# Optimization experiments

Hardware: AMD Instinct MI355X
Metric: run time of the kernel (lower is better)

## Reference

```python
import jax, jax.numpy as jnp
import numpy as np

NW = 64        # n_waveshapers
CE = 128       # control_embedding_size
W = 16         # shaping_fn_size (width)
OC = 1         # out_channels
EPS = 1e-5
SLOPE = 0.01   # LeakyReLU negative slope


def _layer_norm_c(x, g, b):
    # layer norm over channel axis of [B, C, T] (TimeDistributedLayerNorm)
    mu = jnp.mean(x, axis=1, keepdims=True)
    var = jnp.var(x, axis=1, keepdims=True)
    xn = (x - mu) * jax.lax.rsqrt(var + EPS)
    return xn * g[None, :, None] + b[None, :, None]


def _linear_interp(x, out_len):
    # torch F.interpolate(mode='linear', align_corners=False) on [B, C, L]
    L = x.shape[-1]
    scale = L / out_len
    pos = (jnp.arange(out_len, dtype=x.dtype) + 0.5) * scale - 0.5
    pos = jnp.clip(pos, 0.0, L - 1)
    i0 = jnp.floor(pos).astype(jnp.int32)
    i1 = jnp.minimum(i0 + 1, L - 1)
    frac = (pos - i0.astype(x.dtype))
    return x[..., i0] * (1.0 - frac) + x[..., i1] * frac


def setup_inputs() -> dict:
    key = jax.random.key(0)
    ks = jax.random.split(key, 32)
    B, T, TC = 4, 65536, 1024
    s_ce = 1.0 / np.sqrt(CE)
    inp = {
        'exciter': jax.random.normal(ks[0], (B, NW, T), jnp.float32),
        'control_embedding': jax.random.normal(ks[1], (B, CE, TC), jnp.float32),
        # TimeDistributedMLP (depth=4): three CE->CE convs + final CE->4*NW
        'mlp_w0': jax.random.normal(ks[2], (CE, CE), jnp.float32) * s_ce,
        'mlp_b0': jnp.zeros((CE,), jnp.float32),
        'ln0_g': jnp.ones((CE,), jnp.float32),
        'ln0_b': jnp.zeros((CE,), jnp.float32),
        'mlp_w1': jax.random.normal(ks[3], (CE, CE), jnp.float32) * s_ce,
        'mlp_b1': jnp.zeros((CE,), jnp.float32),
        'ln1_g': jnp.ones((CE,), jnp.float32),
        'ln1_b': jnp.zeros((CE,), jnp.float32),
        'mlp_w2': jax.random.normal(ks[4], (CE, CE), jnp.float32) * s_ce,
        'mlp_b2': jnp.zeros((CE,), jnp.float32),
        'ln2_g': jnp.ones((CE,), jnp.float32),
        'ln2_b': jnp.zeros((CE,), jnp.float32),
        'mlp_w3': jax.random.normal(ks[5], (4 * NW, CE), jnp.float32) * s_ce,
        'mlp_b3': jnp.zeros((4 * NW,), jnp.float32),
        # TrainableNonlinearity: input_scale + grouped k=1 convs (per-channel MLPs)
        'input_scale': jax.random.normal(ks[6], (1, NW, 1), jnp.float32) * 10.0,
        'sf_w0': jax.random.normal(ks[7], (NW, W), jnp.float32),            # 1 -> W per group
        'sf_b0': jnp.zeros((NW, W), jnp.float32),
        'sf_w1': jax.random.normal(ks[8], (NW, W, W), jnp.float32) / np.sqrt(W),  # W -> W per group
        'sf_b1': jnp.zeros((NW, W), jnp.float32),
        'sf_w2': jax.random.normal(ks[9], (NW, W), jnp.float32) / np.sqrt(W),     # W -> 1 per group
        'sf_b2': jnp.zeros((NW,), jnp.float32),
        # mixer conv1d NW -> OC, k=1
        'mix_w': jax.random.normal(ks[10], (OC, NW), jnp.float32) / np.sqrt(NW),
        'mix_b': jnp.zeros((OC,), jnp.float32),
    }
    return inp


def reference(exciter, control_embedding,
              mlp_w0, mlp_b0, ln0_g, ln0_b,
              mlp_w1, mlp_b1, ln1_g, ln1_b,
              mlp_w2, mlp_b2, ln2_g, ln2_b,
              mlp_w3, mlp_b3,
              input_scale, sf_w0, sf_b0, sf_w1, sf_b1, sf_w2, sf_b2,
              mix_w, mix_b):
    T = exciter.shape[-1]

    # --- TimeDistributedMLP: (Conv1x1 -> LN(channels) -> LeakyReLU) x3 -> Conv1x1
    h = jnp.einsum('bct,oc->bot', control_embedding, mlp_w0) + mlp_b0[None, :, None]
    h = jax.nn.leaky_relu(_layer_norm_c(h, ln0_g, ln0_b), SLOPE)
    h = jnp.einsum('bct,oc->bot', h, mlp_w1) + mlp_b1[None, :, None]
    h = jax.nn.leaky_relu(_layer_norm_c(h, ln1_g, ln1_b), SLOPE)
    h = jnp.einsum('bct,oc->bot', h, mlp_w2) + mlp_b2[None, :, None]
    h = jax.nn.leaky_relu(_layer_norm_c(h, ln2_g, ln2_b), SLOPE)
    film = jnp.einsum('bct,oc->bot', h, mlp_w3) + mlp_b3[None, :, None]  # [B, 4*NW, TC]

    # upsample control params to audio rate
    film = _linear_interp(film, T)  # [B, 4*NW, T]
    gamma_i, beta_i, gamma_n, beta_n = jnp.split(film, 4, axis=1)

    # FiLM waveshaping index
    x = gamma_i * exciter + beta_i  # [B, NW, T]

    # TrainableNonlinearity: per-channel 1->W->W->1 MLP, Sine activations
    x = input_scale * x
    h0 = jnp.sin(x[:, :, None, :] * sf_w0[None, :, :, None] + sf_b0[None, :, :, None])  # [B,NW,W,T]
    h1 = jnp.sin(jnp.einsum('bcit,coi->bcot', h0, sf_w1) + sf_b1[None, :, :, None])     # [B,NW,W,T]
    x = jnp.sin(jnp.einsum('bcit,ci->bct', h1, sf_w2) + sf_b2[None, :, None])           # [B,NW,T]

    # FiLM normalising coeff
    x = gamma_n * x + beta_n

    # nearest upsample x4 then 1x1 mixer conv
    x = jnp.repeat(x, 4, axis=-1)  # [B, NW, 4T]
    out = jnp.einsum('bct,oc->bot', x, mix_w) + mix_b[None, :, None]  # [B, OC, 4T]
    return out
```

## Files before the change

### kernel.cpp

```cpp
#include <hip/hip_runtime.h>
#include <stdint.h>

#define NB 4
#define NWS 64
#define TT 65536
#define TCC 1024
#define CEE 128
#define WW 16

#define INV2PI 0.15915494309189535f

#define OFF_FILM  0
#define OFF_W0S   (OFF_FILM + NB*256*TCC)
#define OFF_B0S   (OFF_W0S + 1024)
#define OFF_B1S   (OFF_B0S + 1024)
#define OFF_B2S   (OFF_B1S + 1024)
#define OFF_MIX   (OFF_B2S + 64)
#define OFF_AFRAG (OFF_MIX + 64)
#define OFF_A2F   (OFF_AFRAG + 8192)
#define OFF_PART  (OFF_A2F + 8192)

typedef _Float16 half4_t __attribute__((ext_vector_type(4)));
typedef float f32x4_t __attribute__((ext_vector_type(4)));

__device__ __forceinline__ float sinrev(float r) {
#if __has_builtin(__builtin_amdgcn_fractf) && __has_builtin(__builtin_amdgcn_sinf)
  return __builtin_amdgcn_sinf(__builtin_amdgcn_fractf(r));
#else
  float fr = r - floorf(r);
  return __sinf(fr * 6.283185307179586f);
#endif
}

__global__ __launch_bounds__(256) void k_prep(
    const float* __restrict__ iscale,
    const float* __restrict__ w0, const float* __restrict__ b0,
    const float* __restrict__ w1, const float* __restrict__ b1,
    const float* __restrict__ w2, const float* __restrict__ b2,
    const float* __restrict__ mixw,
    float* __restrict__ ws) {
  int i = blockIdx.x * 256 + threadIdx.x;
  if (i < NWS * WW) {
    int n = i / WW;
    ws[OFF_W0S + i] = w0[i] * iscale[n] * INV2PI;
    ws[OFF_B0S + i] = b0[i] * INV2PI;
    ws[OFF_B1S + i] = b1[i] * INV2PI;
  }
  if (i < NWS) {
    ws[OFF_B2S + i] = b2[i] * INV2PI;
    ws[OFF_MIX + i] = mixw[i];
  }
  if (i < NWS * 64) {
    int n = i >> 6, l = i & 63;
    int m = l & 15, k0 = (l >> 4) * 4;
    union { uint2 u; half4_t h; } cv;
    #pragma unroll
    for (int j = 0; j < 4; ++j)
      cv.h[j] = (_Float16)(w1[(n * 16 + m) * 16 + k0 + j] * INV2PI);
    ((uint2*)(ws + OFF_AFRAG))[i] = cv.u;
    union { uint2 u; half4_t h; } c2;
    #pragma unroll
    for (int j = 0; j < 4; ++j)
      c2.h[j] = (_Float16)(w2[n * 16 + k0 + j] * INV2PI);
    ((uint2*)(ws + OFF_A2F))[i] = c2.u;
  }
}

#define MCOLS 8
__global__ __launch_bounds__(256) void k_mlp(
    const float* __restrict__ ce,
    const float* __restrict__ w0, const float* __restrict__ b0,
    const float* __restrict__ g0, const float* __restrict__ e0,
    const float* __restrict__ w1, const float* __restrict__ b1,
    const float* __restrict__ g1, const float* __restrict__ e1,
    const float* __restrict__ w2, const float* __restrict__ b2,
    const float* __restrict__ g2, const float* __restrict__ e2,
    const float* __restrict__ w3, const float* __restrict__ b3,
    float* __restrict__ film) {
  const int tid = threadIdx.x;
  const int o = tid & 127;
  const int h = tid >> 7;
  const int wvid = tid >> 6;
  const int bx = blockIdx.x;
  const int b = bx >> 7;
  const int tc0 = (bx & 127) * MCOLS;

  __shared__ float wlds[128 * 65];
  __shared__ __align__(16) float xa[CEE * MCOLS];
  __shared__ __align__(16) float xb[CEE * MCOLS];
  __shared__ float red[4][2][4];
  __shared__ float stat[2][MCOLS];

  if (tid < 128) {
    const float* src = ce + ((size_t)(b * CEE + tid)) * TCC + tc0;
    *(float4*)(xa + tid * MCOLS) = *(const float4*)src;
    *(float4*)(xa + tid * MCOLS + 4) = *(const float4*)(src + 4);
  }

  float* xin = xa; float* xout = xb;
  const float* Wp[3] = {w0, w1, w2};
  const float* Bp[3] = {b0, b1, b2};
  const float* Gp[3] = {g0, g1, g2};
  const float* Ep[3] = {e0, e1, e2};

  for (int L = 0; L < 3; ++L) {
    float acc[4];
    float bias = Bp[L][o];
    #pragma unroll
    for (int cc = 0; cc < 4; ++cc) acc[cc] = bias;

    for (int half = 0; half < 2; ++half) {
      __syncthreads();
      const float* wsrc = Wp[L] + half * 64;
      for (int i = tid; i < 4096; i += 256) {
        int oo = i >> 5, cc2 = (i & 31) * 2;
        float2 wv = *(const float2*)(wsrc + (size_t)oo * CEE + cc2);
        wlds[oo * 65 + cc2] = wv.x;
        wlds[oo * 65 + cc2 + 1] = wv.y;
      }
      __syncthreads();
      const float* xcol = xin + half * 64 * MCOLS + h * 4;
      const float* wr = wlds + o * 65;
      #pragma unroll 8
      for (int c = 0; c < 64; ++c) {
        float w = wr[c];
        float4 xv = *(const float4*)(xcol + c * MCOLS);
        acc[0] = fmaf(w, xv.x, acc[0]); acc[1] = fmaf(w, xv.y, acc[1]);
        acc[2] = fmaf(w, xv.z, acc[2]); acc[3] = fmaf(w, xv.w, acc[3]);
      }
    }

    float s[4], q[4];
    #pragma unroll
    for (int cc = 0; cc < 4; ++cc) { s[cc] = acc[cc]; q[cc] = acc[cc] * acc[cc]; }
    #pragma unroll
    for (int m = 1; m < 64; m <<= 1) {
      #pragma unroll
      for (int cc = 0; cc < 4; ++cc) {
        s[cc] += __shfl_xor(s[cc], m, 64);
        q[cc] += __shfl_xor(q[cc], m, 64);
      }
    }
    if ((tid & 63) == 0) {
      #pragma unroll
      for (int cc = 0; cc < 4; ++cc) { red[wvid][0][cc] = s[cc]; red[wvid][1][cc] = q[cc]; }
    }
    __syncthreads();
    if (tid < MCOLS) {
      int hh = tid >> 2, cc = tid & 3;
      float st = red[2 * hh][0][cc] + red[2 * hh + 1][0][cc];
      float qt = red[2 * hh][1][cc] + red[2 * hh + 1][1][cc];
      float mu = st * (1.0f / CEE);
      float var = qt * (1.0f / CEE) - mu * mu;
      stat[0][tid] = mu;
      stat[1][tid] = rsqrtf(var + 1e-5f);
    }
    __syncthreads();
    float g = Gp[L][o], e = Ep[L][o];
    #pragma unroll
    for (int cc = 0; cc < 4; ++cc) {
      int col = h * 4 + cc;
      float v = (acc[cc] - stat[0][col]) * stat[1][col] * g + e;
      v = fmaxf(v, 0.01f * v);
      xout[o * MCOLS + col] = v;
    }
    float* tmp = xin; xin = xout; xout = tmp;
  }

  for (int hh = 0; hh < 2; ++hh) {
    float acc[4];
    float bias = b3[hh * 128 + o];
    #pragma unroll
    for (int cc = 0; cc < 4; ++cc) acc[cc] = bias;
    for (int half = 0; half < 2; ++half) {
      __syncthreads();
      const float* wsrc = w3 + (size_t)hh * 128 * CEE + half * 64;
      for (int i = tid; i < 4096; i += 256) {
        int oo = i >> 5, cc2 = (i & 31) * 2;
        float2 wv = *(const float2*)(wsrc + (size_t)oo * CEE + cc2);
        wlds[oo * 65 + cc2] = wv.x;
        wlds[oo * 65 + cc2 + 1] = wv.y;
      }
      __syncthreads();
      const float* xcol = xin + half * 64 * MCOLS + h * 4;
      const float* wr = wlds + o * 65;
      #pragma unroll 8
      for (int c = 0; c < 64; ++c) {
        float w = wr[c];
        float4 xv = *(const float4*)(xcol + c * MCOLS);
        acc[0] = fmaf(w, xv.x, acc[0]); acc[1] = fmaf(w, xv.y, acc[1]);
        acc[2] = fmaf(w, xv.z, acc[2]); acc[3] = fmaf(w, xv.w, acc[3]);
      }
    }
    float* dst = film + ((size_t)(b * 256 + hh * 128 + o)) * TCC + tc0 + h * 4;
    *(float4*)dst = *(float4*)acc;
  }
}

__global__ __launch_bounds__(256, 8) void k_shape(
    const float* __restrict__ exciter,
    const float* __restrict__ ws,
    float* __restrict__ part) {
  const int tid = threadIdx.x;
  const int lane = tid & 63;
  const int wv = tid >> 6;
  const int bx = blockIdx.x;
  const int blk = bx & 255;
  const int b = (bx >> 8) & 3;
  const int half = bx >> 10;
  const int n0 = half * 32;
  const int t0_blk = blk * 256;
  const int tcbase = blk * 4 - 1;

  __shared__ float FL[32 * 24];
  __shared__ __align__(16) float W0s[32 * 16], B0s[32 * 16], B1s[32 * 16];
  __shared__ float BMs[32 * 2];

  for (int i = tid; i < 512; i += 256) {
    W0s[i] = ws[OFF_W0S + n0 * 16 + i];
    B0s[i] = ws[OFF_B0S + n0 * 16 + i];
    B1s[i] = ws[OFF_B1S + n0 * 16 + i];
  }
  if (tid < 64) {
    int n = tid >> 1;
    BMs[tid] = (tid & 1) ? ws[OFF_MIX + n0 + n] : ws[OFF_B2S + n0 + n];
  }
  for (int i = tid; i < 768; i += 256) {
    int n = i / 24, r = i - n * 24, p = r / 6, j = r - p * 6;
    int tc = tcbase + j; tc = tc < 0 ? 0 : (tc > 1023 ? 1023 : tc);
    FL[i] = ws[OFF_FILM + ((size_t)(b * 256 + p * 64 + n0 + n)) * TCC + tc];
  }
  __syncthreads();

  const int t_own = t0_blk + wv * 64 + lane;
  float pos = ((float)t_own + 0.5f) * (1.0f / 64.0f) - 0.5f;
  pos = fminf(fmaxf(pos, 0.0f), 1023.0f);
  float fi = floorf(pos);
  int i0 = (int)fi;
  const float frac = pos - fi;
  const int j0 = i0 - tcbase;

  const int quad = lane >> 4;
  const int l16 = lane & 15;

  float acc = 0.0f;
  const float* excp = exciter + ((size_t)(b * NWS + n0)) * TT + t_own;
  const uint2* af1p = (const uint2*)(ws + OFF_AFRAG) + (size_t)n0 * 64 + lane;
  const uint2* af2p = (const uint2*)(ws + OFF_A2F) + (size_t)n0 * 64 + lane;

  float ev = excp[0];
  uint2 af1 = af1p[0];
  uint2 af2 = af2p[0];
  for (int n = 0; n < 32; ++n) {
    float ev_n = 0.f; uint2 af1_n = af1, af2_n = af2;
    if (n < 31) {
      ev_n = excp[(size_t)(n + 1) * TT];
      af1_n = af1p[(n + 1) * 64];
      af2_n = af2p[(n + 1) * 64];
    }
    const float* fb = FL + n * 24;
    const float* pgi = fb + j0;
    const float* pbi = fb + 6 + j0;
    const float* pgn = fb + 12 + j0;
    const float* pbn = fb + 18 + j0;
    float gi0 = pgi[0], gi = fmaf(pgi[1] - gi0, frac, gi0);
    float bi0 = pbi[0], bi = fmaf(pbi[1] - bi0, frac, bi0);
    float gn0 = pgn[0], gn = fmaf(pgn[1] - gn0, frac, gn0);
    float bn0 = pbn[0], bn = fmaf(pbn[1] - bn0, frac, bn0);
    float x = fmaf(gi, ev, bi);

    f32x4_t w0f = *(const f32x4_t*)(W0s + n * 16 + quad * 4);
    f32x4_t b0f = *(const f32x4_t*)(B0s + n * 16 + quad * 4);
    f32x4_t b1f = *(const f32x4_t*)(B1s + n * 16 + quad * 4);
    float b2v = BMs[n * 2], mwv = BMs[n * 2 + 1];
    half4_t a1, a2;
    { union { uint2 u; half4_t h; } cv; cv.u = af1; a1 = cv.h; }
    { union { uint2 u; half4_t h; } cv; cv.u = af2; a2 = cv.h; }
    f32x4_t c2; c2[0] = b2v; c2[1] = b2v; c2[2] = b2v; c2[3] = b2v;

    float yown = 0.0f;
    #pragma unroll
    for (int g = 0; g < 4; ++g) {
      float xg = __shfl(x, g * 16 + l16, 64);
      half4_t bf1;
      #pragma unroll
      for (int k = 0; k < 4; ++k)
        bf1[k] = (_Float16)sinrev(fmaf(xg, w0f[k], b0f[k]));
      f32x4_t d1 = __builtin_amdgcn_mfma_f32_16x16x16f16(a1, bf1, b1f, 0, 0, 0);
      half4_t bf2;
      #pragma unroll
      for (int k = 0; k < 4; ++k)
        bf2[k] = (_Float16)sinrev(d1[k]);
      f32x4_t d2 = __builtin_amdgcn_mfma_f32_16x16x16f16(a2, bf2, c2, 0, 0, 0);
      yown = (quad == g) ? d2[0] : yown;
    }
    float z = sinrev(yown);
    acc = fmaf(mwv, fmaf(gn, z, bn), acc);
    ev = ev_n; af1 = af1_n; af2 = af2_n;
  }
  part[((size_t)(half * NB + b)) * TT + t_own] = acc;
}

__global__ __launch_bounds__(256) void k_mix(
    const float* __restrict__ part,
    const float* __restrict__ mixb,
    float* __restrict__ out) {
  int i = blockIdx.x * 256 + threadIdx.x;
  float s = part[i] + part[NB * TT + i] + mixb[0];
  float4 v = {s, s, s, s};
  *(float4*)(out + 4 * (size_t)i) = v;
}

extern "C" void kernel_launch(void* const* d_in, const int* in_sizes, int n_in,
                              void* d_out, int out_size, void* d_ws, size_t ws_size,
                              hipStream_t stream) {
  const float* exciter = (const float*)d_in[0];
  const float* ce      = (const float*)d_in[1];
  const float* w0  = (const float*)d_in[2];
  const float* b0  = (const float*)d_in[3];
  const float* g0  = (const float*)d_in[4];
  const float* e0  = (const float*)d_in[5];
  const float* w1  = (const float*)d_in[6];
  const float* b1  = (const float*)d_in[7];
  const float* g1  = (const float*)d_in[8];
  const float* e1  = (const float*)d_in[9];
  const float* w2  = (const float*)d_in[10];
  const float* b2  = (const float*)d_in[11];
  const float* g2  = (const float*)d_in[12];
  const float* e2  = (const float*)d_in[13];
  const float* w3  = (const float*)d_in[14];
  const float* b3  = (const float*)d_in[15];
  const float* iscale = (const float*)d_in[16];
  const float* sw0 = (const float*)d_in[17];
  const float* sb0 = (const float*)d_in[18];
  const float* sw1 = (const float*)d_in[19];
  const float* sb1 = (const float*)d_in[20];
  const float* sw2 = (const float*)d_in[21];
  const float* sb2 = (const float*)d_in[22];
  const float* mixw = (const float*)d_in[23];
  const float* mixb = (const float*)d_in[24];

  float* ws = (float*)d_ws;

  hipLaunchKernelGGL(k_prep, dim3(16), dim3(256), 0, stream,
                     iscale, sw0, sb0, sw1, sb1, sw2, sb2, mixw, ws);
  hipLaunchKernelGGL(k_mlp, dim3(512), dim3(256), 0, stream,
                     ce, w0, b0, g0, e0, w1, b1, g1, e1, w2, b2, g2, e2, w3, b3,
                     ws + OFF_FILM);
  hipLaunchKernelGGL(k_shape, dim3(2048), dim3(256), 0, stream,
                     exciter, ws, ws + OFF_PART);
  hipLaunchKernelGGL(k_mix, dim3(1024), dim3(256), 0, stream,
                     ws + OFF_PART, mixb, (float*)d_out);
}
```

Measured before the change: 261.3 us.

## Precompute FiLM slopes, fold mixer weights into FiLM, merge weight fragments, widen mix

In the shaping kernel, the FiLM parameters are repacked in shared memory as (value, slope) pairs, and the mixer weight is folded into the normalising gamma. The mixer-weighted beta_n is summed once per block and added at the end, so each waveshaper step needs three interpolations instead of four plus a separate multiply. The two MFMA weight fragments are merged into one 16-byte load per step, and the b2 bias is added before the final sine instead of being passed as the MFMA accumulator. The mix kernel now processes four samples per thread with vector loads. These changes cut per-iteration LDS reads and ALU work in the hot loop, at the cost of extra prep work and two more barriers per block.

```diff
diff --git a/kernel.cpp b/kernel.cpp
--- a/kernel.cpp
+++ b/kernel.cpp
@@ -17,8 +17,7 @@
 #define OFF_B2S   (OFF_B1S + 1024)
 #define OFF_MIX   (OFF_B2S + 64)
 #define OFF_AFRAG (OFF_MIX + 64)
-#define OFF_A2F   (OFF_AFRAG + 8192)
-#define OFF_PART  (OFF_A2F + 8192)
+#define OFF_PART  (OFF_AFRAG + 16384)
 
 typedef _Float16 half4_t __attribute__((ext_vector_type(4)));
 typedef float f32x4_t __attribute__((ext_vector_type(4)));
@@ -57,12 +56,12 @@
     #pragma unroll
     for (int j = 0; j < 4; ++j)
       cv.h[j] = (_Float16)(w1[(n * 16 + m) * 16 + k0 + j] * INV2PI);
-    ((uint2*)(ws + OFF_AFRAG))[i] = cv.u;
     union { uint2 u; half4_t h; } c2;
     #pragma unroll
     for (int j = 0; j < 4; ++j)
       c2.h[j] = (_Float16)(w2[n * 16 + k0 + j] * INV2PI);
-    ((uint2*)(ws + OFF_A2F))[i] = c2.u;
+    uint4 o; o.x = cv.u.x; o.y = cv.u.y; o.z = c2.u.x; o.w = c2.u.y;
+    ((uint4*)(ws + OFF_AFRAG))[i] = o;
   }
 }
 
@@ -212,23 +211,44 @@
   const int t0_blk = blk * 256;
   const int tcbase = blk * 4 - 1;
 
-  __shared__ float FL[32 * 24];
+  __shared__ float FLraw[32 * 24];
+  __shared__ float FLp[32 * 36];
+  __shared__ float Sraw[8], Spair[12];
   __shared__ __align__(16) float W0s[32 * 16], B0s[32 * 16], B1s[32 * 16];
-  __shared__ float BMs[32 * 2];
+  __shared__ float B2s[32], MWs[32];
 
   for (int i = tid; i < 512; i += 256) {
     W0s[i] = ws[OFF_W0S + n0 * 16 + i];
     B0s[i] = ws[OFF_B0S + n0 * 16 + i];
     B1s[i] = ws[OFF_B1S + n0 * 16 + i];
   }
-  if (tid < 64) {
-    int n = tid >> 1;
-    BMs[tid] = (tid & 1) ? ws[OFF_MIX + n0 + n] : ws[OFF_B2S + n0 + n];
+  if (tid < 32) {
+    B2s[tid] = ws[OFF_B2S + n0 + tid];
+    MWs[tid] = ws[OFF_MIX + n0 + tid];
   }
   for (int i = tid; i < 768; i += 256) {
     int n = i / 24, r = i - n * 24, p = r / 6, j = r - p * 6;
     int tc = tcbase + j; tc = tc < 0 ? 0 : (tc > 1023 ? 1023 : tc);
-    FL[i] = ws[OFF_FILM + ((size_t)(b * 256 + p * 64 + n0 + n)) * TCC + tc];
+    FLraw[i] = ws[OFF_FILM + ((size_t)(b * 256 + p * 64 + n0 + n)) * TCC + tc];
+  }
+  __syncthreads();
+  for (int i = tid; i < 576; i += 256) {
+    int n = i / 18, r = i - n * 18, p = r / 6, j = r - p * 6;
+    float v = FLraw[n * 24 + p * 6 + j];
+    float vn = (j < 5) ? FLraw[n * 24 + p * 6 + j + 1] : v;
+    float sc = (p == 2) ? MWs[n] : 1.0f;
+    FLp[n * 36 + p * 12 + 2 * j] = v * sc;
+    FLp[n * 36 + p * 12 + 2 * j + 1] = (vn - v) * sc;
+  }
+  if (tid < 6) {
+    float s = 0.0f;
+    for (int n = 0; n < 32; ++n) s += MWs[n] * FLraw[n * 24 + 18 + tid];
+    Sraw[tid] = s;
+  }
+  __syncthreads();
+  if (tid < 6) {
+    Spair[2 * tid] = Sraw[tid];
+    Spair[2 * tid + 1] = (tid < 5) ? Sraw[tid + 1] - Sraw[tid] : 0.0f;
   }
   __syncthreads();
 
@@ -245,38 +265,34 @@
 
   float acc = 0.0f;
   const float* excp = exciter + ((size_t)(b * NWS + n0)) * TT + t_own;
-  const uint2* af1p = (const uint2*)(ws + OFF_AFRAG) + (size_t)n0 * 64 + lane;
-  const uint2* af2p = (const uint2*)(ws + OFF_A2F) + (size_t)n0 * 64 + lane;
+  const uint4* afp = (const uint4*)(ws + OFF_AFRAG) + (size_t)n0 * 64 + lane;
+
+  f32x4_t czero; czero[0] = 0.f; czero[1] = 0.f; czero[2] = 0.f; czero[3] = 0.f;
 
   float ev = excp[0];
-  uint2 af1 = af1p[0];
-  uint2 af2 = af2p[0];
+  uint4 af = afp[0];
   for (int n = 0; n < 32; ++n) {
-    float ev_n = 0.f; uint2 af1_n = af1, af2_n = af2;
+    float ev_n = 0.f; uint4 af_n = af;
     if (n < 31) {
       ev_n = excp[(size_t)(n + 1) * TT];
-      af1_n = af1p[(n + 1) * 64];
-      af2_n = af2p[(n + 1) * 64];
-    }
-    const float* fb = FL + n * 24;
-    const float* pgi = fb + j0;
-    const float* pbi = fb + 6 + j0;
-    const float* pgn = fb + 12 + j0;
-    const float* pbn = fb + 18 + j0;
-    float gi0 = pgi[0], gi = fmaf(pgi[1] - gi0, frac, gi0);
-    float bi0 = pbi[0], bi = fmaf(pbi[1] - bi0, frac, bi0);
-    float gn0 = pgn[0], gn = fmaf(pgn[1] - gn0, frac, gn0);
-    float bn0 = pbn[0], bn = fmaf(pbn[1] - bn0, frac, bn0);
+      af_n = afp[(n + 1) * 64];
+    }
+    const float* fp = FLp + n * 36 + 2 * j0;
+    float2 gp = *(const float2*)(fp);
+    float2 bp = *(const float2*)(fp + 12);
+    float2 np = *(const float2*)(fp + 24);
+    float gi = fmaf(gp.y, frac, gp.x);
+    float bi = fmaf(bp.y, frac, bp.x);
+    float gnp = fmaf(np.y, frac, np.x);
     float x = fmaf(gi, ev, bi);
 
     f32x4_t w0f = *(const f32x4_t*)(W0s + n * 16 + quad * 4);
     f32x4_t b0f = *(const f32x4_t*)(B0s + n * 16 + quad * 4);
     f32x4_t b1f = *(const f32x4_t*)(B1s + n * 16 + quad * 4);
-    float b2v = BMs[n * 2], mwv = BMs[n * 2 + 1];
+    float b2v = B2s[n];
     half4_t a1, a2;
-    { union { uint2 u; half4_t h; } cv; cv.u = af1; a1 = cv.h; }
-    { union { uint2 u; half4_t h; } cv; cv.u = af2; a2 = cv.h; }
-    f32x4_t c2; c2[0] = b2v; c2[1] = b2v; c2[2] = b2v; c2[3] = b2v;
+    { union { uint2 u; half4_t h; } cv; cv.u.x = af.x; cv.u.y = af.y; a1 = cv.h; }
+    { union { uint2 u; half4_t h; } cv; cv.u.x = af.z; cv.u.y = af.w; a2 = cv.h; }
 
     float yown = 0.0f;
     #pragma unroll
@@ -291,24 +307,31 @@
       #pragma unroll
       for (int k = 0; k < 4; ++k)
         bf2[k] = (_Float16)sinrev(d1[k]);
-      f32x4_t d2 = __builtin_amdgcn_mfma_f32_16x16x16f16(a2, bf2, c2, 0, 0, 0);
+      f32x4_t d2 = __builtin_amdgcn_mfma_f32_16x16x16f16(a2, bf2, czero, 0, 0, 0);
       yown = (quad == g) ? d2[0] : yown;
     }
-    float z = sinrev(yown);
-    acc = fmaf(mwv, fmaf(gn, z, bn), acc);
-    ev = ev_n; af1 = af1_n; af2 = af2_n;
-  }
-  part[((size_t)(half * NB + b)) * TT + t_own] = acc;
+    float z = sinrev(yown + b2v);
+    acc = fmaf(gnp, z, acc);
+    ev = ev_n; af = af_n;
+  }
+  float2 sp = *(const float2*)(Spair + 2 * j0);
+  part[((size_t)(half * NB + b)) * TT + t_own] = acc + fmaf(sp.y, frac, sp.x);
 }
 
 __global__ __launch_bounds__(256) void k_mix(
     const float* __restrict__ part,
     const float* __restrict__ mixb,
     float* __restrict__ out) {
-  int i = blockIdx.x * 256 + threadIdx.x;
-  float s = part[i] + part[NB * TT + i] + mixb[0];
-  float4 v = {s, s, s, s};
-  *(float4*)(out + 4 * (size_t)i) = v;
+  int idx = blockIdx.x * 256 + threadIdx.x;
+  float m = mixb[0];
+  float4 a = ((const float4*)part)[idx];
+  float4 c = ((const float4*)(part + NB * TT))[idx];
+  float4* o = (float4*)(out + (size_t)idx * 16);
+  float s0 = a.x + c.x + m, s1 = a.y + c.y + m, s2 = a.z + c.z + m, s3 = a.w + c.w + m;
+  o[0] = make_float4(s0, s0, s0, s0);
+  o[1] = make_float4(s1, s1, s1, s1);
+  o[2] = make_float4(s2, s2, s2, s2);
+  o[3] = make_float4(s3, s3, s3, s3);
 }
 
 extern "C" void kernel_launch(void* const* d_in, const int* in_sizes, int n_in,
@@ -349,6 +372,6 @@
                      ws + OFF_FILM);
   hipLaunchKernelGGL(k_shape, dim3(2048), dim3(256), 0, stream,
                      exciter, ws, ws + OFF_PART);
-  hipLaunchKernelGGL(k_mix, dim3(1024), dim3(256), 0, stream,
+  hipLaunchKernelGGL(k_mix, dim3(256), dim3(256), 0, stream,
                      ws + OFF_PART, mixb, (float*)d_out);
 }
```

After: 258.7 us. Within noise of the previous version (-1.0%).
